# Kernel optimization log

Hardware: AMD Instinct MI355X
Metric: run time of the kernel (lower is better)

Reference implementation:

```python
import jax, jax.numpy as jnp
import numpy as np

NUM_HEADS = 16
D_MODEL = 1024
HEAD_DIM = D_MODEL // NUM_HEADS
EMB = 1024
B, L = 2, 2048


def setup_inputs() -> dict:
    key = jax.random.key(0)
    k1, k2, k3 = jax.random.split(key, 3)
    scale_in = 1.0 / np.sqrt(EMB)
    scale_out = 1.0 / np.sqrt(D_MODEL)
    return {
        "x": jax.random.normal(k1, (B, L, EMB), dtype=jnp.float32),
        "W_qkv": jax.random.normal(k2, (EMB, 3 * D_MODEL), dtype=jnp.float32) * scale_in,
        "b_qkv": jnp.zeros((3 * D_MODEL,), dtype=jnp.float32),
        "W_out": jax.random.normal(k3, (D_MODEL, EMB), dtype=jnp.float32) * scale_out,
        "b_out": jnp.zeros((EMB,), dtype=jnp.float32),
    }


def reference(x, W_qkv, b_qkv, W_out, b_out):
    Bn, Ln, _ = x.shape
    qkv = x @ W_qkv + b_qkv  # [B, L, 3*d_model]
    q = qkv[:, :, :D_MODEL].reshape(Bn, Ln, NUM_HEADS, HEAD_DIM)
    k = qkv[:, :, D_MODEL:2 * D_MODEL].reshape(Bn, Ln, NUM_HEADS, HEAD_DIM)
    v = qkv[:, :, 2 * D_MODEL:].reshape(Bn, Ln, NUM_HEADS, HEAD_DIM)
    scores = jnp.einsum('bqhd,bkhd->bhqk', q, k)  # [B, H, L, L]
    attn = jax.nn.softmax(scores / jnp.sqrt(jnp.float32(HEAD_DIM)), axis=-1)
    out = jnp.einsum('bhqk,bkhd->bqhd', attn, v).reshape(Bn, Ln, D_MODEL)
    return out @ W_out + b_out
```

## Files before the change

### kernel.cpp

```cpp
#include <hip/hip_runtime.h>
#include <stdint.h>

#define B_   2
#define L_   2048
#define H_   16
#define D_   64
#define EMB_ 1024
#define DM_  1024
#define N3_  3072
#define TOK_ 4096

typedef unsigned short u16;
typedef unsigned int u32;
typedef __attribute__((ext_vector_type(4))) float f32x4;
typedef __attribute__((ext_vector_type(8))) short s16x8;
typedef __attribute__((ext_vector_type(4))) u32 u32x4;
typedef __attribute__((ext_vector_type(2))) u32 u32x2;
typedef __attribute__((ext_vector_type(4))) u16 u16x4;

#define MFMA(a,b,c) __builtin_amdgcn_mfma_f32_16x16x32_bf16(a,b,c,0,0,0)

#define AS1 __attribute__((address_space(1)))
#define AS3 __attribute__((address_space(3)))
#define GLLDS(g, l) __builtin_amdgcn_global_load_lds( \
    (const AS1 u32*)(const void*)(g), (AS3 u32*)(void*)(l), 16, 0, 0)

#define QSCALE 0.18033688011f

static __device__ __forceinline__ u16 f2bf(float f) {
  u32 u = __builtin_bit_cast(u32, f);
  u = (u + 0x7fffu + ((u >> 16) & 1u)) >> 16;
  return (u16)u;
}

static __device__ __forceinline__ u32 pack2bf(float a, float b) {
#if __has_builtin(__builtin_amdgcn_cvt_pk_bf16_f32)
  auto v = __builtin_amdgcn_cvt_pk_bf16_f32(a, b);
  return __builtin_bit_cast(u32, v);
#else
  return (u32)f2bf(a) | ((u32)f2bf(b) << 16);
#endif
}

static __device__ __forceinline__ float fexp2(float x) {
#if __has_builtin(__builtin_amdgcn_exp2f)
  return __builtin_amdgcn_exp2f(x);
#else
  float r;
  asm("v_exp_f32 %0, %1" : "=v"(r) : "v"(x));
  return r;
#endif
}

__global__ __launch_bounds__(256) void k_prep(
    const float* __restrict__ x,   u16* __restrict__ xb,
    const float* __restrict__ Wq,  u16* __restrict__ wqT,
    const float* __restrict__ Wo,  u16* __restrict__ woT)
{
  const int blk = blockIdx.x, tid = threadIdx.x;
  if (blk < 4096) {
    int i = (blk * 256 + tid) * 4;
    float4 v = *(const float4*)(x + i);
    ushort4 o;
    o.x = f2bf(v.x); o.y = f2bf(v.y); o.z = f2bf(v.z); o.w = f2bf(v.w);
    *(ushort4*)(xb + i) = o;
    return;
  }
  __shared__ float tile[32][33];
  const float* in;
  u16* out;
  int R, C, bx, by;
  if (blk < 4096 + 3072) {
    int t = blk - 4096;
    in = Wq; out = wqT; R = EMB_; C = N3_;
    bx = t % 96; by = t / 96;
  } else {
    int t = blk - 7168;
    in = Wo; out = woT; R = DM_; C = DM_;
    bx = t & 31; by = t >> 5;
  }
  int c0 = bx * 32, r0 = by * 32;
  int tx = tid & 31, ty = tid >> 5;
  #pragma unroll
  for (int i = 0; i < 32; i += 8)
    tile[ty + i][tx] = in[(size_t)(r0 + ty + i) * C + (c0 + tx)];
  __syncthreads();
  #pragma unroll
  for (int i = 0; i < 32; i += 8)
    out[(size_t)(c0 + ty + i) * R + (r0 + tx)] = f2bf(tile[tx][ty + i]);
}

template<int EPI>
__global__ __launch_bounds__(256, 2) void k_gemm(
    const u16* __restrict__ A, const u16* __restrict__ Bt,
    const float* __restrict__ bias, int M, int N, int K,
    float* __restrict__ Cf,
    u16* __restrict__ Qo, u16* __restrict__ Ko, u16* __restrict__ Vo)
{
  const int tid = threadIdx.x;
  const int wave = tid >> 6, lane = tid & 63;
  const int lr = lane & 15, lk = lane >> 4;
  const int wr = wave >> 1, wc = wave & 1;
  const int m0 = blockIdx.y * 128, n0 = blockIdx.x * 128;

  __shared__ u16 As[128 * 32];
  __shared__ u16 Bs[128 * 32];

  f32x4 acc[4][4] = {};

  const int srow = wave * 32 + (lane >> 2);
  const int schunk = (lane & 3) * 8;
  const u16* gA0 = A  + (size_t)(m0 + srow) * K + schunk;
  const u16* gB0 = Bt + (size_t)(n0 + srow) * K + schunk;
  const u16* gA1 = gA0 + (size_t)16 * K;
  const u16* gB1 = gB0 + (size_t)16 * K;
  u16* lA = As + wave * (32 * 32);
  u16* lB = Bs + wave * (32 * 32);

  for (int k0 = 0; k0 < K; k0 += 32) {
    __syncthreads();
    GLLDS(gA0 + k0, lA);
    GLLDS(gA1 + k0, lA + 16 * 32);
    GLLDS(gB0 + k0, lB);
    GLLDS(gB1 + k0, lB + 16 * 32);
    __syncthreads();

    s16x8 af[4], bf[4];
    #pragma unroll
    for (int mi = 0; mi < 4; ++mi)
      af[mi] = *(const s16x8*)(As + (wr * 64 + mi * 16 + lr) * 32 + lk * 8);
    #pragma unroll
    for (int ni = 0; ni < 4; ++ni)
      bf[ni] = *(const s16x8*)(Bs + (wc * 64 + ni * 16 + lr) * 32 + lk * 8);
    #pragma unroll
    for (int mi = 0; mi < 4; ++mi)
      #pragma unroll
      for (int ni = 0; ni < 4; ++ni)
        acc[mi][ni] = MFMA(af[mi], bf[ni], acc[mi][ni]);
  }

  const int mbase = m0 + wr * 64 + lk * 4;
  #pragma unroll
  for (int ni = 0; ni < 4; ++ni) {
    int gn = n0 + wc * 64 + ni * 16 + lr;
    float bz = bias[gn];
    #pragma unroll
    for (int mi = 0; mi < 4; ++mi) {
      #pragma unroll
      for (int r = 0; r < 4; ++r) {
        int gm = mbase + mi * 16 + r;
        float v = acc[mi][ni][r] + bz;
        if (EPI == 1) {
          Cf[(size_t)gm * N + gn] = v;
        } else {
          int sec = gn >> 10, cm = gn & 1023;
          int h = cm >> 6, d = cm & 63;
          int b = gm >> 11, l = gm & 2047;
          int bh = b * H_ + h;
          if (sec == 0)      Qo[((size_t)bh * L_ + l) * D_ + d] = f2bf(v * QSCALE);
          else if (sec == 1) Ko[((size_t)bh * L_ + l) * D_ + d] = f2bf(v);
          else               Vo[((size_t)bh * D_ + d) * L_ + l] = f2bf(v);
        }
      }
    }
  }
}

__global__ __launch_bounds__(256, 4) void k_flash(
    const u16* __restrict__ Q, const u16* __restrict__ Kb,
    const u16* __restrict__ Vt, u16* __restrict__ AO)
{
  const int tid = threadIdx.x;
  const int wave = tid >> 6, lane = tid & 63;
  const int lr = lane & 15, lk = lane >> 4;
  const int qt = blockIdx.x, bh = blockIdx.y;
  const int b = bh >> 4, h = bh & 15;
  const u16* Qh = Q  + (size_t)bh * L_ * D_;
  const u16* Kh = Kb + (size_t)bh * L_ * D_;
  const u16* Vh = Vt + (size_t)bh * D_ * L_;

  __shared__ u16 Ks[64 * 72];
  __shared__ u16 Vs[64 * 72];
  __shared__ u16 Ps[64 * 72];

  const int qrow0 = qt * 64 + wave * 16;
  s16x8 qf[2];
  #pragma unroll
  for (int ks = 0; ks < 2; ++ks)
    qf[ks] = *(const s16x8*)(Qh + (size_t)(qrow0 + lr) * D_ + ks * 32 + lk * 8);

  f32x4 acco[4] = {};
  float lst = 0.f;

  u16* Pw = Ps + (wave * 16) * 72;

  for (int t0 = 0; t0 < L_; t0 += 64) {
    __syncthreads();
    #pragma unroll
    for (int t = 0; t < 2; ++t) {
      int idx = t * 256 + tid;
      int row = idx >> 3, c8 = (idx & 7) * 8;
      u32x4 kv = *(const u32x4*)(Kh + (size_t)(t0 + row) * D_ + c8);
      u32x4 vv = *(const u32x4*)(Vh + (size_t)row * L_ + t0 + c8);
      *(u32x4*)(Ks + row * 72 + c8) = kv;
      *(u32x4*)(Vs + row * 72 + c8) = vv;
    }
    __syncthreads();

    f32x4 accs[4] = {};
    s16x8 kf[4][2];
    #pragma unroll
    for (int mi = 0; mi < 4; ++mi)
      #pragma unroll
      for (int ks = 0; ks < 2; ++ks)
        kf[mi][ks] = *(const s16x8*)(Ks + (mi * 16 + lr) * 72 + ks * 32 + lk * 8);
    #pragma unroll
    for (int mi = 0; mi < 4; ++mi) {
      accs[mi] = MFMA(kf[mi][0], qf[0], accs[mi]);
      accs[mi] = MFMA(kf[mi][1], qf[1], accs[mi]);
    }

    #pragma unroll
    for (int mi = 0; mi < 4; ++mi) {
      float p0 = fexp2(accs[mi][0]);
      float p1 = fexp2(accs[mi][1]);
      float p2 = fexp2(accs[mi][2]);
      float p3 = fexp2(accs[mi][3]);
      lst += (p0 + p1) + (p2 + p3);
      u32x2 pk = { pack2bf(p0, p1), pack2bf(p2, p3) };
      *(u32x2*)(Pw + lr * 72 + mi * 16 + lk * 4) = pk;
    }

    s16x8 vf[4][2], pf[2];
    #pragma unroll
    for (int di = 0; di < 4; ++di)
      #pragma unroll
      for (int ks = 0; ks < 2; ++ks)
        vf[di][ks] = *(const s16x8*)(Vs + (di * 16 + lr) * 72 + ks * 32 + lk * 8);
    #pragma unroll
    for (int ks = 0; ks < 2; ++ks)
      pf[ks] = *(const s16x8*)(Pw + lr * 72 + ks * 32 + lk * 8);
    #pragma unroll
    for (int di = 0; di < 4; ++di) {
      acco[di] = MFMA(vf[di][0], pf[0], acco[di]);
      acco[di] = MFMA(vf[di][1], pf[1], acco[di]);
    }
  }

  lst += __shfl_xor(lst, 16);
  lst += __shfl_xor(lst, 32);
  float rl = 1.0f / lst;
  const int q = qrow0 + lr;
  #pragma unroll
  for (int di = 0; di < 4; ++di) {
    u16x4 o;
    #pragma unroll
    for (int r = 0; r < 4; ++r)
      o[r] = f2bf(acco[di][r] * rl);
    *(u16x4*)(AO + (size_t)(b * L_ + q) * DM_ + h * D_ + di * 16 + lk * 4) = o;
  }
}

extern "C" void kernel_launch(void* const* d_in, const int* in_sizes, int n_in,
                              void* d_out, int out_size, void* d_ws, size_t ws_size,
                              hipStream_t stream)
{
  const float* x    = (const float*)d_in[0];
  const float* Wqkv = (const float*)d_in[1];
  const float* bqkv = (const float*)d_in[2];
  const float* Wout = (const float*)d_in[3];
  const float* bout = (const float*)d_in[4];
  float* out = (float*)d_out;

  u16* xb  = (u16*)d_ws;
  u16* wqT = xb  + (size_t)TOK_ * EMB_;
  u16* woT = wqT + (size_t)N3_ * EMB_;
  u16* qb  = woT + (size_t)DM_ * EMB_;
  u16* kb  = qb  + (size_t)B_ * H_ * L_ * D_;
  u16* vt  = kb  + (size_t)B_ * H_ * L_ * D_;
  u16* ao  = vt  + (size_t)B_ * H_ * L_ * D_;

  k_prep<<<4096 + 3072 + 1024, 256, 0, stream>>>(x, xb, Wqkv, wqT, Wout, woT);
  k_gemm<0><<<dim3(N3_ / 128, TOK_ / 128), 256, 0, stream>>>(
      xb, wqT, bqkv, TOK_, N3_, EMB_, nullptr, qb, kb, vt);
  k_flash<<<dim3(L_ / 64, B_ * H_), 256, 0, stream>>>(qb, kb, vt, ao);
  k_gemm<1><<<dim3(DM_ / 128, TOK_ / 128), 256, 0, stream>>>(
      ao, woT, bout, TOK_, DM_, EMB_, out, nullptr, nullptr, nullptr);
}
```

Before: 213.4 us.

## Double-buffer K/V tiles via async global-to-LDS loads with XOR swizzle and XCD-aware block mapping

The flash-attention kernel now prefetches the next K and V tiles straight into a second LDS buffer with global_load_lds while the current tile is computed, and drops one of the two barriers per iteration. The padded LDS rows are replaced by an XOR-swizzled unpadded layout for K, V and P to avoid bank conflicts. Blocks are remapped from a 2D grid to a 1D grid so that blocks sharing a head land on the same XCD for L2 reuse. The cost is more LDS per block and a swizzle that must match exactly between the load, store and read sides.

```diff
diff --git a/kernel.cpp b/kernel.cpp
--- a/kernel.cpp
+++ b/kernel.cpp
@@ -173,15 +173,18 @@
   const int tid = threadIdx.x;
   const int wave = tid >> 6, lane = tid & 63;
   const int lr = lane & 15, lk = lane >> 4;
-  const int qt = blockIdx.x, bh = blockIdx.y;
+  const int blk = blockIdx.x;
+  const int idx = blk >> 3;
+  const int bh = (blk & 7) * 4 + (idx >> 5);
+  const int qt = idx & 31;
   const int b = bh >> 4, h = bh & 15;
   const u16* Qh = Q  + (size_t)bh * L_ * D_;
   const u16* Kh = Kb + (size_t)bh * L_ * D_;
   const u16* Vh = Vt + (size_t)bh * D_ * L_;
 
-  __shared__ u16 Ks[64 * 72];
-  __shared__ u16 Vs[64 * 72];
-  __shared__ u16 Ps[64 * 72];
+  __shared__ u16 Ks[2][64 * 64];
+  __shared__ u16 Vs[2][64 * 64];
+  __shared__ u16 Ps[64 * 64];
 
   const int qrow0 = qt * 64 + wave * 16;
   s16x8 qf[2];
@@ -192,28 +195,45 @@
   f32x4 acco[4] = {};
   float lst = 0.f;
 
-  u16* Pw = Ps + (wave * 16) * 72;
-
-  for (int t0 = 0; t0 < L_; t0 += 64) {
+  const int srow0 = wave * 16 + (lane >> 3);
+  const int gch8 = (((lane & 7) ^ ((lane >> 3) & 7)) * 8);
+  u16* kd0 = (u16*)Ks[0] + wave * (16 * 64);
+  u16* kd1 = (u16*)Ks[1] + wave * (16 * 64);
+  u16* vd0 = (u16*)Vs[0] + wave * (16 * 64);
+  u16* vd1 = (u16*)Vs[1] + wave * (16 * 64);
+
+  const int ck0 = (lk ^ (lr & 7)) * 8;
+  const int sxor = (lr & 7) << 1;
+  u16* PsW = Ps + wave * (16 * 64);
+
+  GLLDS(Kh + (size_t)srow0 * 64 + gch8,        kd0);
+  GLLDS(Kh + (size_t)(srow0 + 8) * 64 + gch8,  kd0 + 8 * 64);
+  GLLDS(Vh + (size_t)srow0 * L_ + gch8,        vd0);
+  GLLDS(Vh + (size_t)(srow0 + 8) * L_ + gch8,  vd0 + 8 * 64);
+
+  int buf = 0;
+  for (int t0 = 0; t0 < L_; t0 += 64, buf ^= 1) {
     __syncthreads();
-    #pragma unroll
-    for (int t = 0; t < 2; ++t) {
-      int idx = t * 256 + tid;
-      int row = idx >> 3, c8 = (idx & 7) * 8;
-      u32x4 kv = *(const u32x4*)(Kh + (size_t)(t0 + row) * D_ + c8);
-      u32x4 vv = *(const u32x4*)(Vh + (size_t)row * L_ + t0 + c8);
-      *(u32x4*)(Ks + row * 72 + c8) = kv;
-      *(u32x4*)(Vs + row * 72 + c8) = vv;
-    }
-    __syncthreads();
-
+
+    if (t0 + 64 < L_) {
+      const int tn = t0 + 64;
+      u16* kd = buf ? kd0 : kd1;
+      u16* vd = buf ? vd0 : vd1;
+      GLLDS(Kh + (size_t)(tn + srow0) * 64 + gch8,       kd);
+      GLLDS(Kh + (size_t)(tn + srow0 + 8) * 64 + gch8,   kd + 8 * 64);
+      GLLDS(Vh + ((size_t)srow0 * L_ + tn + gch8),       vd);
+      GLLDS(Vh + ((size_t)(srow0 + 8) * L_ + tn + gch8), vd + 8 * 64);
+    }
+
+    const u16* Kbuf = (const u16*)Ks[buf];
     f32x4 accs[4] = {};
     s16x8 kf[4][2];
     #pragma unroll
-    for (int mi = 0; mi < 4; ++mi)
-      #pragma unroll
-      for (int ks = 0; ks < 2; ++ks)
-        kf[mi][ks] = *(const s16x8*)(Ks + (mi * 16 + lr) * 72 + ks * 32 + lk * 8);
+    for (int mi = 0; mi < 4; ++mi) {
+      const u16* rp = Kbuf + (mi * 16 + lr) * 64;
+      kf[mi][0] = *(const s16x8*)(rp + ck0);
+      kf[mi][1] = *(const s16x8*)(rp + (ck0 ^ 32));
+    }
     #pragma unroll
     for (int mi = 0; mi < 4; ++mi) {
       accs[mi] = MFMA(kf[mi][0], qf[0], accs[mi]);
@@ -228,18 +248,19 @@
       float p3 = fexp2(accs[mi][3]);
       lst += (p0 + p1) + (p2 + p3);
       u32x2 pk = { pack2bf(p0, p1), pack2bf(p2, p3) };
-      *(u32x2*)(Pw + lr * 72 + mi * 16 + lk * 4) = pk;
-    }
-
+      *(u32x2*)(PsW + lr * 64 + (((4 * mi + lk) ^ sxor) * 4)) = pk;
+    }
+
+    const u16* Vbuf = (const u16*)Vs[buf];
     s16x8 vf[4][2], pf[2];
     #pragma unroll
-    for (int di = 0; di < 4; ++di)
-      #pragma unroll
-      for (int ks = 0; ks < 2; ++ks)
-        vf[di][ks] = *(const s16x8*)(Vs + (di * 16 + lr) * 72 + ks * 32 + lk * 8);
-    #pragma unroll
-    for (int ks = 0; ks < 2; ++ks)
-      pf[ks] = *(const s16x8*)(Pw + lr * 72 + ks * 32 + lk * 8);
+    for (int di = 0; di < 4; ++di) {
+      const u16* rp = Vbuf + (di * 16 + lr) * 64;
+      vf[di][0] = *(const s16x8*)(rp + ck0);
+      vf[di][1] = *(const s16x8*)(rp + (ck0 ^ 32));
+    }
+    pf[0] = *(const s16x8*)(PsW + lr * 64 + (((2 * lk) ^ sxor) * 4));
+    pf[1] = *(const s16x8*)(PsW + lr * 64 + (((8 + 2 * lk) ^ sxor) * 4));
     #pragma unroll
     for (int di = 0; di < 4; ++di) {
       acco[di] = MFMA(vf[di][0], pf[0], acco[di]);
@@ -283,7 +304,7 @@
   k_prep<<<4096 + 3072 + 1024, 256, 0, stream>>>(x, xb, Wqkv, wqT, Wout, woT);
   k_gemm<0><<<dim3(N3_ / 128, TOK_ / 128), 256, 0, stream>>>(
       xb, wqT, bqkv, TOK_, N3_, EMB_, nullptr, qb, kb, vt);
-  k_flash<<<dim3(L_ / 64, B_ * H_), 256, 0, stream>>>(qb, kb, vt, ao);
+  k_flash<<<1024, 256, 0, stream>>>(qb, kb, vt, ao);
   k_gemm<1><<<dim3(DM_ / 128, TOK_ / 128), 256, 0, stream>>>(
       ao, woT, bout, TOK_, DM_, EMB_, out, nullptr, nullptr, nullptr);
 }
```

Measured after the change: 205.9 us. -3.5%, faster.
